# Performance work log

Measured on AMD Instinct MI355X. Metric: run time of the kernel, lower is better.

## Reference

```python
import jax, jax.numpy as jnp
import numpy as np

B, T, DIM = 1, 1024, 1024
H = 8
QLR, KVLR = 768, 512
DNOPE, DROPE, DV = 128, 64, 128
DK = DNOPE + DROPE  # 192
EPS = 1e-5


def _rms(x, w):
    return x * jax.lax.rsqrt(jnp.mean(x * x, axis=-1, keepdims=True) + EPS) * w


def _l2norm(x):
    return x * jax.lax.rsqrt(jnp.sum(x * x, axis=-1, keepdims=True) + 1e-6)


def setup_inputs() -> dict:
    key = jax.random.key(0)
    ks = jax.random.split(key, 12)
    std = 0.02
    rnd = lambda k, shape: (jax.random.normal(k, shape, dtype=jnp.float32) * std)
    return {
        'x': jax.random.normal(ks[0], (B, T, DIM), dtype=jnp.float32),
        'cos': jax.random.normal(ks[1], (T, DROPE), dtype=jnp.float32),
        'sin': jax.random.normal(ks[2], (T, DROPE), dtype=jnp.float32),
        'wq_a': rnd(ks[3], (DIM, QLR)),
        'q_norm_w': jnp.ones((QLR,), dtype=jnp.float32),
        'wq_b': rnd(ks[4], (QLR, H * DK)),
        'wkv_a': rnd(ks[5], (DIM, KVLR + DROPE)),
        'kv_norm_w': jnp.ones((KVLR,), dtype=jnp.float32),
        'wkv_b': rnd(ks[6], (KVLR, H * (DNOPE + DV))),
        'wg_w': rnd(ks[7], (DIM, H * DK)),
        'wg_b': jnp.zeros((H * DK,), dtype=jnp.float32),
        'wb': rnd(ks[8], (DIM, H)),
        'wo': rnd(ks[9], (H * DV, DIM)),
    }


def _kda(q, k, v, g, beta):
    # q,k: [B,T,H,DK]; v: [B,T,H,DV]; g: [B,T,H,DK] (log-decay); beta: [B,T,H]
    q = _l2norm(q) * (DK ** -0.5)
    k = _l2norm(k)
    # time-major for scan
    qs = jnp.moveaxis(q, 1, 0)
    ks_ = jnp.moveaxis(k, 1, 0)
    vs = jnp.moveaxis(v, 1, 0)
    gs = jnp.moveaxis(g, 1, 0)
    bs = jnp.moveaxis(beta, 1, 0)

    def step(S, inp):
        q_t, k_t, v_t, g_t, b_t = inp  # [B,H,DK],[B,H,DK],[B,H,DV],[B,H,DK],[B,H]
        S = S * jnp.exp(g_t)[..., None]                       # per-key-dim decay
        u_t = b_t[..., None] * (v_t - jnp.einsum('bhk,bhkv->bhv', k_t, S))
        S = S + k_t[..., None] * u_t[..., None, :]            # rank-1 delta update
        o_t = jnp.einsum('bhk,bhkv->bhv', q_t, S)
        return S, o_t

    S0 = jnp.zeros((B, H, DK, DV), dtype=q.dtype)
    _, o = jax.lax.scan(step, S0, (qs, ks_, vs, gs, bs))
    return jnp.moveaxis(o, 0, 1)  # [B,T,H,DV]


def reference(x, cos, sin, wq_a, q_norm_w, wq_b, wkv_a, kv_norm_w, wkv_b, wg_w, wg_b, wb, wo):
    # cos/sin are accepted but unused, matching the original forward body.
    q = (_rms(x @ wq_a, q_norm_w) @ wq_b).reshape(B, T, H, DK)
    kv_all = x @ wkv_a
    kv_c, k_pe = kv_all[..., :KVLR], kv_all[..., KVLR:]       # [B,T,KVLR],[B,T,DROPE]
    kv = (_rms(kv_c, kv_norm_w) @ wkv_b).reshape(B, T, H, DNOPE + DV)
    k_nope, v = kv[..., :DNOPE], kv[..., DNOPE:]
    k = jnp.concatenate(
        [k_nope, jnp.broadcast_to(k_pe[:, :, None, :], (B, T, H, DROPE))], axis=-1)
    g = jax.nn.log_sigmoid(x @ wg_w + wg_b).reshape(B, T, H, DK)
    beta = jax.nn.sigmoid(x @ wb).reshape(B, T, H)
    o = _kda(q, k, v, g, beta)
    o = jnp.nan_to_num(o, nan=0.0, posinf=10000.0, neginf=-10000.0)
    return o.reshape(B, T, H * DV) @ wo
```

## Files before the change

### kernel.cpp

```cpp
#include <hip/hip_runtime.h>
#include <hip/hip_bf16.h>
#include <math.h>

#define TT 1024
#define DIM 1024
#define HH 8
#define QLR 768
#define KVLR 512
#define DNOPE 128
#define DROPE 64
#define DV 128
#define DK 192
#define HDK (HH*DK)
#define HKV (HH*(DNOPE+DV))

#define OY   0
#define OQ   3072
#define OC   6144
#define OPL  9984
#define OU   10240
#define OLAM 12288
#define PABLK 12480

typedef __attribute__((ext_vector_type(8))) short short8;
typedef __attribute__((ext_vector_type(4))) float f32x4;

__device__ __forceinline__ unsigned short f2bf_rn(float f) {
    unsigned u = __float_as_uint(f);
    unsigned lsb = (u >> 16) & 1u;
    u += 0x7fffu + lsb;
    return (unsigned short)(u >> 16);
}
__device__ __forceinline__ float bf2f(unsigned short h) {
    return __uint_as_float(((unsigned)h) << 16);
}

__global__ __launch_bounds__(256) void wconv(
    const float* __restrict__ W0, unsigned short* __restrict__ H0,
    unsigned short* __restrict__ L0, int K0, int N0, int T0,
    const float* __restrict__ W1, unsigned short* __restrict__ H1,
    unsigned short* __restrict__ L1, int K1, int N1, int T1,
    const float* __restrict__ W2, unsigned short* __restrict__ H2,
    unsigned short* __restrict__ L2, int K2, int N2, int T2)
{
    __shared__ float Ls[64][65];
    int bx = blockIdx.x;
    const float* W; unsigned short* H; unsigned short* L; int K, N;
    if (bx < T0)           { W = W0; H = H0; L = L0; K = K0; N = N0; }
    else if (bx < T0 + T1) { bx -= T0; W = W1; H = H1; L = L1; K = K1; N = N1; }
    else                   { bx -= T0 + T1; W = W2; H = H2; L = L2; K = K2; N = N2; }

    const int NT = N >> 6;
    const int kt = bx / NT, nt = bx - kt * NT;
    const int k0 = kt * 64, n0 = nt * 64;
    const int tid = threadIdx.x;
    const int r = tid >> 2, c = (tid & 3) * 16;

#pragma unroll
    for (int i = 0; i < 4; i++)
        *(float4*)&Ls[r][c + i * 4] =
            *(const float4*)&W[(size_t)(k0 + r) * N + n0 + c + i * 4];
    __syncthreads();

    const int nr = tid >> 2, kc = (tid & 3) * 16;
    unsigned short hb[16], lb[16];
#pragma unroll
    for (int j = 0; j < 16; j++) {
        float v = Ls[kc + j][nr];
        unsigned short h = f2bf_rn(v);
        hb[j] = h;
        lb[j] = f2bf_rn(v - bf2f(h));
    }
    size_t ob = (size_t)(n0 + nr) * K + k0 + kc;
    *(float4*)&H[ob]     = ((float4*)hb)[0];
    *(float4*)&H[ob + 8] = ((float4*)hb)[1];
    *(float4*)&L[ob]     = ((float4*)lb)[0];
    *(float4*)&L[ob + 8] = ((float4*)lb)[1];
}

__global__ __launch_bounds__(256) void aconv(
    const float* __restrict__ A, unsigned short* __restrict__ H,
    unsigned short* __restrict__ L)
{
    int i = (blockIdx.x * 256 + threadIdx.x) * 8;
    float4 v0 = *(const float4*)&A[i];
    float4 v1 = *(const float4*)&A[i + 4];
    float vv[8] = {v0.x, v0.y, v0.z, v0.w, v1.x, v1.y, v1.z, v1.w};
    unsigned short hb[8], lb[8];
#pragma unroll
    for (int j = 0; j < 8; j++) {
        unsigned short h = f2bf_rn(vv[j]);
        hb[j] = h;
        lb[j] = f2bf_rn(vv[j] - bf2f(h));
    }
    *(float4*)&H[i] = *(float4*)hb;
    *(float4*)&L[i] = *(float4*)lb;
}

__global__ __launch_bounds__(128) void gemm_bt(
    const unsigned short* __restrict__ Ah0, const unsigned short* __restrict__ Al0,
    const unsigned short* __restrict__ Bh0, const unsigned short* __restrict__ Bl0,
    float* __restrict__ C0, int K0, int N0, int T0,
    const unsigned short* __restrict__ Ah1, const unsigned short* __restrict__ Al1,
    const unsigned short* __restrict__ Bh1, const unsigned short* __restrict__ Bl1,
    float* __restrict__ C1, int K1, int N1, int T1,
    const unsigned short* __restrict__ Ah2, const unsigned short* __restrict__ Al2,
    const unsigned short* __restrict__ Bh2, const unsigned short* __restrict__ Bl2,
    float* __restrict__ C2, int K2, int N2, int T2)
{
    __shared__ unsigned short Ahs[64 * 40], Als[64 * 40];
    __shared__ unsigned short Bhs[64 * 40], Bls[64 * 40];

    int bx = blockIdx.x;
    const unsigned short *Ah, *Al, *Bh, *Bl; float* C; int K, N;
    if (bx < T0) {
        Ah = Ah0; Al = Al0; Bh = Bh0; Bl = Bl0; C = C0; K = K0; N = N0;
    } else if (bx < T0 + T1) {
        bx -= T0; Ah = Ah1; Al = Al1; Bh = Bh1; Bl = Bl1; C = C1; K = K1; N = N1;
    } else {
        bx -= T0 + T1; Ah = Ah2; Al = Al2; Bh = Bh2; Bl = Bl2; C = C2; K = K2; N = N2;
    }

    const int tid = threadIdx.x;
    const int w = tid >> 6, l = tid & 63;
    const int q = l >> 4, m16 = l & 15;
    const int bm = blockIdx.y * 64, bn = bx * 64;

    const int c0i = tid * 2, c1i = tid * 2 + 1;
    const int r0 = c0i >> 2, o0 = (c0i & 3) * 8;
    const int r1 = c1i >> 2, o1 = (c1i & 3) * 8;
    const unsigned short* pAh0 = Ah + (size_t)(bm + r0) * K + o0;
    const unsigned short* pAh1 = Ah + (size_t)(bm + r1) * K + o1;
    const unsigned short* pAl0 = Al + (size_t)(bm + r0) * K + o0;
    const unsigned short* pAl1 = Al + (size_t)(bm + r1) * K + o1;
    const unsigned short* pBh0 = Bh + (size_t)(bn + r0) * K + o0;
    const unsigned short* pBh1 = Bh + (size_t)(bn + r1) * K + o1;
    const unsigned short* pBl0 = Bl + (size_t)(bn + r0) * K + o0;
    const unsigned short* pBl1 = Bl + (size_t)(bn + r1) * K + o1;

    f32x4 acc[2][4];
#pragma unroll
    for (int i = 0; i < 2; i++)
#pragma unroll
        for (int j = 0; j < 4; j++)
            acc[i][j] = (f32x4){0.f, 0.f, 0.f, 0.f};

    float4 vAh0 = *(const float4*)pAh0, vAh1 = *(const float4*)pAh1;
    float4 vAl0 = *(const float4*)pAl0, vAl1 = *(const float4*)pAl1;
    float4 vBh0 = *(const float4*)pBh0, vBh1 = *(const float4*)pBh1;
    float4 vBl0 = *(const float4*)pBl0, vBl1 = *(const float4*)pBl1;

    for (int k0 = 0;; k0 += 32) {
        __syncthreads();
        *(float4*)&Ahs[r0 * 40 + o0] = vAh0; *(float4*)&Ahs[r1 * 40 + o1] = vAh1;
        *(float4*)&Als[r0 * 40 + o0] = vAl0; *(float4*)&Als[r1 * 40 + o1] = vAl1;
        *(float4*)&Bhs[r0 * 40 + o0] = vBh0; *(float4*)&Bhs[r1 * 40 + o1] = vBh1;
        *(float4*)&Bls[r0 * 40 + o0] = vBl0; *(float4*)&Bls[r1 * 40 + o1] = vBl1;
        __syncthreads();

        const bool more = (k0 + 32) < K;
        if (more) {
            const int kn = k0 + 32;
            vAh0 = *(const float4*)(pAh0 + kn); vAh1 = *(const float4*)(pAh1 + kn);
            vAl0 = *(const float4*)(pAl0 + kn); vAl1 = *(const float4*)(pAl1 + kn);
            vBh0 = *(const float4*)(pBh0 + kn); vBh1 = *(const float4*)(pBh1 + kn);
            vBl0 = *(const float4*)(pBl0 + kn); vBl1 = *(const float4*)(pBl1 + kn);
        }

        short8 fah[2], fal[2], fbh[4], fbl[4];
#pragma unroll
        for (int mt = 0; mt < 2; mt++) {
            const int row = w * 32 + mt * 16 + m16;
            fah[mt] = *(const short8*)&Ahs[row * 40 + q * 8];
            fal[mt] = *(const short8*)&Als[row * 40 + q * 8];
        }
#pragma unroll
        for (int nt = 0; nt < 4; nt++) {
            const int row = nt * 16 + m16;
            fbh[nt] = *(const short8*)&Bhs[row * 40 + q * 8];
            fbl[nt] = *(const short8*)&Bls[row * 40 + q * 8];
        }
#pragma unroll
        for (int mt = 0; mt < 2; mt++)
#pragma unroll
            for (int nt = 0; nt < 4; nt++) {
                acc[mt][nt] = __builtin_amdgcn_mfma_f32_16x16x32_bf16(
                    fah[mt], fbh[nt], acc[mt][nt], 0, 0, 0);
                acc[mt][nt] = __builtin_amdgcn_mfma_f32_16x16x32_bf16(
                    fah[mt], fbl[nt], acc[mt][nt], 0, 0, 0);
                acc[mt][nt] = __builtin_amdgcn_mfma_f32_16x16x32_bf16(
                    fal[mt], fbh[nt], acc[mt][nt], 0, 0, 0);
            }
        if (!more) break;
    }

#pragma unroll
    for (int mt = 0; mt < 2; mt++)
#pragma unroll
        for (int nt = 0; nt < 4; nt++) {
            const int mrow = bm + w * 32 + mt * 16 + q * 4;
            const int ncol = bn + nt * 16 + m16;
#pragma unroll
            for (int r = 0; r < 4; r++)
                C[(size_t)(mrow + r) * N + ncol] = acc[mt][nt][r];
        }
}

__global__ __launch_bounds__(256) void rmsnorm_bf2(
    const float* __restrict__ in0, const float* __restrict__ w0,
    unsigned short* __restrict__ oh0, unsigned short* __restrict__ ol0,
    const float* __restrict__ in1, const float* __restrict__ w1,
    unsigned short* __restrict__ oh1, unsigned short* __restrict__ ol1)
{
    int bx = blockIdx.x;
    const float* in; const float* w; unsigned short *oh, *ol;
    int t, stride, ncols; float inv_n;
    if (bx < TT) {
        t = bx; in = in0; w = w0; oh = oh0; ol = ol0;
        stride = QLR; ncols = QLR; inv_n = 1.f / QLR;
    } else {
        t = bx - TT; in = in1; w = w1; oh = oh1; ol = ol1;
        stride = KVLR + DROPE; ncols = KVLR; inv_n = 1.f / KVLR;
    }
    const int tid = threadIdx.x;
    const float* row = in + (size_t)t * stride;
    float ss = 0.f;
    for (int c = tid; c < ncols; c += 256) { float v = row[c]; ss += v * v; }
#pragma unroll
    for (int m = 1; m < 64; m <<= 1) ss += __shfl_xor(ss, m);
    __shared__ float red[4];
    if ((tid & 63) == 0) red[tid >> 6] = ss;
    __syncthreads();
    float tot = red[0] + red[1] + red[2] + red[3];
    float scale = rsqrtf(tot * inv_n + 1e-5f);
    for (int c = tid; c < ncols; c += 256) {
        float v = row[c] * scale * w[c];
        unsigned short h = f2bf_rn(v);
        oh[(size_t)t * ncols + c] = h;
        ol[(size_t)t * ncols + c] = f2bf_rn(v - bf2f(h));
    }
}

__global__ __launch_bounds__(256) void small_fused(
    const float* __restrict__ g, const float* __restrict__ bias,
    float* __restrict__ la_h,
    const float* __restrict__ x, const float* __restrict__ wb,
    float* __restrict__ betab,
    const float* __restrict__ qraw, const float* __restrict__ kvb,
    const float* __restrict__ kv_all, float* __restrict__ q_h,
    float* __restrict__ k_h)
{
    int bx = blockIdx.x;
    if (bx < 6144) {
        int i = bx * 256 + threadIdx.x;
        int t = i / HDK, col = i - t * HDK;
        int h = col / DK, d = col - h * DK;
        float z = g[i] + bias[col];
        float la = fminf(z, 0.f) - log1pf(__expf(-fabsf(z)));
        la_h[((size_t)h * TT + t) * DK + d] = la;
        return;
    }
    bx -= 6144;
    const int lane = threadIdx.x & 63, wv = threadIdx.x >> 6;
    if (bx < 2048) {
        const int p = bx * 4 + wv;
        const int t = p >> 3, h = p & 7;
        const float* xr = x + (size_t)t * DIM;
        float s = 0.f;
        for (int e = lane; e < DIM; e += 64) s += xr[e] * wb[e * HH + h];
#pragma unroll
        for (int m = 1; m < 64; m <<= 1) s += __shfl_xor(s, m);
        if (lane == 0) betab[p] = 1.f / (1.f + expf(-s));
        return;
    }
    bx -= 2048;
    {
        const int p = bx * 4 + wv;
        const int t = p >> 3, h = p & 7;

        const float* qrow = qraw + (size_t)t * HDK + h * DK;
        float q0 = qrow[lane], q1 = qrow[lane + 64], q2 = qrow[lane + 128];
        float ss = q0 * q0 + q1 * q1 + q2 * q2;
#pragma unroll
        for (int m = 1; m < 64; m <<= 1) ss += __shfl_xor(ss, m);
        float sc = rsqrtf(ss + 1e-6f) * 0.07216878364870323f;
        float* qo = q_h + ((size_t)h * TT + t) * DK;
        qo[lane] = q0 * sc; qo[lane + 64] = q1 * sc; qo[lane + 128] = q2 * sc;

        const float* knope = kvb + (size_t)t * HKV + h * (DNOPE + DV);
        float k0 = knope[lane], k1 = knope[lane + 64];
        float k2 = kv_all[(size_t)t * (KVLR + DROPE) + KVLR + lane];
        float ks = k0 * k0 + k1 * k1 + k2 * k2;
#pragma unroll
        for (int m = 1; m < 64; m <<= 1) ks += __shfl_xor(ks, m);
        float kc = rsqrtf(ks + 1e-6f);
        float* ko = k_h + ((size_t)h * TT + t) * DK;
        ko[lane] = k0 * kc; ko[lane + 64] = k1 * kc; ko[lane + 128] = k2 * kc;
    }
}

__device__ __forceinline__ float dpp_xor1(float x) {
    return __int_as_float(__builtin_amdgcn_update_dpp(
        0, __float_as_int(x), 0xB1, 0xF, 0xF, false));
}
__device__ __forceinline__ float dpp_xor2(float x) {
    return __int_as_float(__builtin_amdgcn_update_dpp(
        0, __float_as_int(x), 0x4E, 0xF, 0xF, false));
}
__device__ __forceinline__ float dpp_hm(float x) {
    return __int_as_float(__builtin_amdgcn_update_dpp(
        0, __float_as_int(x), 0x141, 0xF, 0xF, false));
}
__device__ __forceinline__ float red16(float x) {
    x += dpp_xor1(x);
    x += dpp_xor2(x);
    x += dpp_hm(x);
    x += __int_as_float(__builtin_amdgcn_update_dpp(0, __float_as_int(x), 0x140, 0xF, 0xF, false));
    return x;
}

__device__ __forceinline__ void gl_lds16(const float* g, float* l) {
    __builtin_amdgcn_global_load_lds(
        (const __attribute__((address_space(1))) void*)g,
        (__attribute__((address_space(3))) void*)l, 16, 0, 0);
}
__device__ __forceinline__ void gl_lds4(const float* g, float* l) {
    __builtin_amdgcn_global_load_lds(
        (const __attribute__((address_space(1))) void*)g,
        (__attribute__((address_space(3))) void*)l, 4, 0, 0);
}

__global__ __launch_bounds__(256) void chunk_prep(
    const float* __restrict__ k_h, const float* __restrict__ la_h,
    const float* __restrict__ q_h, const float* __restrict__ kvb,
    const float* __restrict__ betab, float* __restrict__ pa)
{
    __shared__ float Ls[16][196];
    __shared__ float Ks[16][196];
    __shared__ float Qs[16][196];
    __shared__ float Ws[16][196];
    __shared__ float Xs[16][196];
    __shared__ float Ms[16][16];
    __shared__ float bs[16];

    const int tid = threadIdx.x;
    const int n = blockIdx.x >> 3, h = blockIdx.x & 7;
    const size_t g0 = ((size_t)h * TT + n * 16) * DK;
    float* blob = pa + (size_t)blockIdx.x * PABLK;

#pragma unroll
    for (int s = 0; s < 3; s++) {
        int off = (tid * 3 + s) * 4;
        int r = off / 192, c = off - r * 192;
        *(float4*)&Ks[r][c] = *(const float4*)(k_h + g0 + off);
        *(float4*)&Ls[r][c] = *(const float4*)(la_h + g0 + off);
        *(float4*)&Qs[r][c] = *(const float4*)(q_h + g0 + off);
    }
    if (tid < 16) bs[tid] = betab[(size_t)(n * 16 + tid) * HH + h];
    __syncthreads();

    if (tid < 192) {
        float g = 0.f;
#pragma unroll
        for (int i = 0; i < 16; i++) { g += Ls[i][tid]; Ls[i][tid] = g; }
    }
    __syncthreads();

#pragma unroll
    for (int s = 0; s < 12; s++) {
        int idx = s * 256 + tid;
        int i = idx / 192, d = idx - i * 192;
        float G = Ls[i][d];
        float eg = __expf(G), en = __expf(-G);
        float kk = Ks[i][d];
        Ws[i][d] = bs[i] * kk * eg;
        Qs[i][d] *= eg;
        Ks[i][d] = kk * en;
    }
    __syncthreads();

#pragma unroll
    for (int s = 0; s < 3; s++) {
        int off = (tid * 3 + s) * 4;
        int r = off / 192, c = off - r * 192;
        *(float4*)(blob + OQ + off) = *(const float4*)&Qs[r][c];
    }
    if (tid < 192) {
        float lam = __expf(Ls[15][tid]);
        blob[OLAM + tid] = lam;
#pragma unroll
        for (int j4 = 0; j4 < 4; j4++) {
            float4 v;
            v.x = Ks[j4 * 4 + 0][tid] * lam; v.y = Ks[j4 * 4 + 1][tid] * lam;
            v.z = Ks[j4 * 4 + 2][tid] * lam; v.w = Ks[j4 * 4 + 3][tid] * lam;
            *(float4*)(blob + OC + tid * 20 + j4 * 4) = v;
        }
        blob[OC + tid * 20 + 16] = lam;
        blob[OC + tid * 20 + 17] = 0.f;
        blob[OC + tid * 20 + 18] = 0.f; blob[OC + tid * 20 + 19] = 0.f;
    }
    {
        const int i = tid >> 4, j = tid & 15;
        float m = 0.f, p = 0.f;
#pragma unroll
        for (int d4 = 0; d4 < 48; d4++) {
            float4 w  = *(const float4*)&Ws[i][d4 * 4];
            float4 ka = *(const float4*)&Ks[j][d4 * 4];
            float4 qa = *(const float4*)&Qs[i][d4 * 4];
            m += w.x * ka.x + w.y * ka.y + w.z * ka.z + w.w * ka.w;
            p += qa.x * ka.x + qa.y * ka.y + qa.z * ka.z + qa.w * ka.w;
        }
        Ms[i][j] = (j < i) ? m : 0.f;
        blob[OPL + tid] = (j <= i) ? p : 0.f;
    }
    __syncthreads();

    float y[16], uu[16];
    const bool doY = (tid < 192);
    const bool doU = (tid >= 128);
    const int dcol = tid, ccol = tid - 128;
    if (doY) {
#pragma unroll
        for (int i = 0; i < 16; i++) y[i] = Ws[i][dcol];
#pragma unroll
        for (int i = 1; i < 16; i++)
#pragma unroll
            for (int j = 0; j < i; j++)
                y[i] = fmaf(-Ms[i][j], y[j], y[i]);
    }
    if (doU) {
#pragma unroll
        for (int i = 0; i < 16; i++)
            uu[i] = bs[i] * kvb[(size_t)(n * 16 + i) * HKV + h * (DNOPE + DV) + DNOPE + ccol];
#pragma unroll
        for (int i = 1; i < 16; i++)
#pragma unroll
            for (int j = 0; j < i; j++)
                uu[i] = fmaf(-Ms[i][j], uu[j], uu[i]);
    }
    if (doY) {
#pragma unroll
        for (int i = 0; i < 16; i++) Xs[i][dcol] = y[i];
    }
    __syncthreads();
#pragma unroll
    for (int s = 0; s < 3; s++) {
        int off = (tid * 3 + s) * 4;
        int r = off / 192, c = off - r * 192;
        *(float4*)(blob + OY + off) = *(const float4*)&Xs[r][c];
    }
    __syncthreads();
    if (doU) {
#pragma unroll
        for (int i = 0; i < 16; i++) Xs[i][ccol] = uu[i];
    }
    __syncthreads();
#pragma unroll
    for (int s = 0; s < 2; s++) {
        int off = (tid * 2 + s) * 4;
        int r = off / 128, c = off - r * 128;
        *(float4*)(blob + OU + off) = *(const float4*)&Xs[r][c];
    }
}

__global__ __launch_bounds__(512, 4) void kda_chunk(
    const float* __restrict__ pa, unsigned short* __restrict__ obh,
    unsigned short* __restrict__ obl)
{
    __shared__ float Cb[3][3840];
    __shared__ float Pb[3][256];
    __shared__ float ubs[3][32];
    __shared__ float lbs[3][192];
    __shared__ float Ss[392];
    __shared__ float us[40];

    const int tid = threadIdx.x;
    const int w = tid >> 6, lane = tid & 63;
    const int h = blockIdx.x & 7, cg = blockIdx.x >> 3;
    const int c0 = cg * 2;

    const int dg  = tid & 15;
    const int cc  = (tid >> 4) & 1;
    const int tig = tid >> 5;
    const int dbase = dg * 12;

    auto stage = [&](int buf, int n) {
        const float* blob = pa + (size_t)(n * 8 + h) * PABLK;
        if (w < 3) {
#pragma unroll
            for (int s = 0; s < 4; s++)
                gl_lds16(blob + OC + (w * 4 + s) * 256 + lane * 4,
                         &Cb[buf][(w * 4 + s) * 256]);
        } else if (w == 3) {
#pragma unroll
            for (int s = 12; s < 15; s++)
                gl_lds16(blob + OC + s * 256 + lane * 4, &Cb[buf][s * 256]);
        } else if (w == 4) {
            gl_lds16(blob + OPL + lane * 4, &Pb[buf][0]);
        } else if (w == 5) {
            if (lane < 32)
                gl_lds4(blob + OU + (lane >> 1) * 128 + c0 + (lane & 1), &ubs[buf][0]);
            if (lane < 48)
                gl_lds16(blob + OLAM + lane * 4, &lbs[buf][0]);
        }
    };

    auto ldYQ = [&](int n, float4 (&Y)[3], float4 (&Q)[3]) {
        const float* blob = pa + (size_t)(n * 8 + h) * PABLK;
        const float* py_ = blob + OY + tig * 192 + dbase;
        const float* pq_ = blob + OQ + tig * 192 + dbase;
#pragma unroll
        for (int s = 0; s < 3; s++) {
            Y[s] = *(const float4*)(py_ + s * 4);
            Q[s] = *(const float4*)(pq_ + s * 4);
        }
    };

    for (int idx = tid; idx < 392; idx += 512) Ss[idx] = 0.f;
    stage(0, 0);
    stage(1, 1);

    float4 YA[3], QA[3], YB[3], QB[3];
    ldYQ(0, YA, QA);

    auto body = [&](int n, int bf, float4 (&Yc)[3], float4 (&Qc)[3],
                    float4 (&Yn)[3], float4 (&Qn)[3]) {
        __syncthreads();

        if (n + 2 < TT / 16) {
            int b2 = bf + 2; if (b2 >= 3) b2 -= 3;
            stage(b2, n + 2);
        }
        {
            int np = n + 1; if (np > TT / 16 - 1) np = TT / 16 - 1;
            ldYQ(np, Yn, Qn);
        }

        float4 sv[3];
#pragma unroll
        for (int s = 0; s < 3; s++)
            sv[s] = *(const float4*)&Ss[cc * 196 + dbase + s * 4];

        float py = 0.f, pq = 0.f;
#pragma unroll
        for (int s = 0; s < 3; s++) {
            float4 yv = Yc[s];
            float4 qv = Qc[s];
            float4 s4 = sv[s];
            py = fmaf(yv.x, s4.x, py);
            py = fmaf(yv.y, s4.y, py);
            py = fmaf(yv.z, s4.z, py);
            py = fmaf(yv.w, s4.w, py);
            pq = fmaf(qv.x, s4.x, pq);
            pq = fmaf(qv.y, s4.y, pq);
            pq = fmaf(qv.z, s4.z, pq);
            pq = fmaf(qv.w, s4.w, pq);
        }
        float zy = red16(py);
        float zq = red16(pq);

        float uv = ubs[bf][tig * 2 + cc] - zy;
        if (dg == 0) us[cc * 20 + tig] = uv;
        __syncthreads();

        {
            float acc = (dg <= tig) ? Pb[bf][tig * 16 + dg] * us[cc * 20 + dg]
                                    : 0.f;
            acc = red16(acc);
            if (dg == 0) {
                float ov = zq + acc;
                if (isnan(ov)) ov = 0.f;
                else if (isinf(ov)) ov = ov > 0.f ? 1e4f : -1e4f;
                size_t oi = (size_t)(n * 16 + tig) * (HH * DV) + h * DV + c0 + cc;
                unsigned short hb = f2bf_rn(ov);
                obh[oi] = hb;
                obl[oi] = f2bf_rn(ov - bf2f(hb));
            }
        }

        if (tid < 384) {
            const int d = tid >> 1, c2 = tid & 1;
            const float4* up = (const float4*)&us[c2 * 20];
            float4 u0 = up[0], u1 = up[1], u2v = up[2], u3 = up[3];
            float svv = Ss[c2 * 196 + d];
            float a2 = lbs[bf][d] * svv;
            const float4* C4 = (const float4*)&Cb[bf][d * 20];
            float4 k0 = C4[0], k1 = C4[1], k2 = C4[2], k3 = C4[3];
            a2 = fmaf(k0.x, u0.x,  a2); a2 = fmaf(k0.y, u0.y,  a2);
            a2 = fmaf(k0.z, u0.z,  a2); a2 = fmaf(k0.w, u0.w,  a2);
            a2 = fmaf(k1.x, u1.x,  a2); a2 = fmaf(k1.y, u1.y,  a2);
            a2 = fmaf(k1.z, u1.z,  a2); a2 = fmaf(k1.w, u1.w,  a2);
            a2 = fmaf(k2.x, u2v.x, a2); a2 = fmaf(k2.y, u2v.y, a2);
            a2 = fmaf(k2.z, u2v.z, a2); a2 = fmaf(k2.w, u2v.w, a2);
            a2 = fmaf(k3.x, u3.x,  a2); a2 = fmaf(k3.y, u3.y,  a2);
            a2 = fmaf(k3.z, u3.z,  a2); a2 = fmaf(k3.w, u3.w,  a2);
            Ss[c2 * 196 + d] = a2;
        }
    };

    int buf = 0;
    for (int n = 0; n < TT / 16; n += 2) {
        body(n, buf, YA, QA, YB, QB);
        int b1 = buf + 1; if (b1 >= 3) b1 -= 3;
        body(n + 1, b1, YB, QB, YA, QA);
        buf += 2; if (buf >= 3) buf -= 3;
    }
}

extern "C" void kernel_launch(void* const* d_in, const int* in_sizes, int n_in,
                              void* d_out, int out_size, void* d_ws, size_t ws_size,
                              hipStream_t stream)
{
    const float* x         = (const float*)d_in[0];
    const float* wq_a      = (const float*)d_in[3];
    const float* q_norm_w  = (const float*)d_in[4];
    const float* wq_b      = (const float*)d_in[5];
    const float* wkv_a     = (const float*)d_in[6];
    const float* kv_norm_w = (const float*)d_in[7];
    const float* wkv_b     = (const float*)d_in[8];
    const float* wg_w      = (const float*)d_in[9];
    const float* wg_b      = (const float*)d_in[10];
    const float* wb        = (const float*)d_in[11];
    const float* wo        = (const float*)d_in[12];
    float* out = (float*)d_out;

    float* ws = (float*)d_ws;
    float* xq     = ws;
    float* kv_all = xq     + TT * QLR;
    float* agraw  = kv_all + TT * (KVLR + DROPE);
    float* qnraw  = agraw  + TT * HDK;
    float* kvb    = qnraw  + TT * HDK;
    float* la_h   = kvb    + TT * HKV;
    float* q_h    = la_h   + TT * HDK;
    float* k_h    = q_h    + TT * HDK;
    float* betab  = k_h    + TT * HDK;
    float* pa     = betab  + TT * HH;
    float* tail   = pa     + 512 * PABLK;

    unsigned short* wo_h  = (unsigned short*)tail;
    unsigned short* wo_l  = wo_h  + 1048576;
    unsigned short* xh    = wo_l  + 1048576;
    unsigned short* xl    = xh    + 1048576;
    unsigned short* xqh   = xl    + 1048576;
    unsigned short* xql   = xqh   + 786432;
    unsigned short* kvnh  = xql   + 786432;
    unsigned short* kvnl  = kvnh  + 524288;

    unsigned short* wqa_h  = (unsigned short*)pa;
    unsigned short* wqa_l  = wqa_h  + 786432;
    unsigned short* wkva_h = wqa_l  + 786432;
    unsigned short* wkva_l = wkva_h + 589824;
    unsigned short* wgw_h  = wkva_l + 589824;
    unsigned short* wgw_l  = wgw_h  + 1572864;
    unsigned short* wqb_h  = wgw_l  + 1572864;
    unsigned short* wqb_l  = wqb_h  + 1179648;
    unsigned short* wkvb_h = wqb_l  + 1179648;
    unsigned short* wkvb_l = wkvb_h + 1048576;

    unsigned short* obh = (unsigned short*)agraw;
    unsigned short* obl = obh + 1048576;

    dim3 blk(256);

    wconv<<<dim3(192 + 144 + 384), blk, 0, stream>>>(
        wq_a, wqa_h, wqa_l, DIM, QLR, 192,
        wkv_a, wkva_h, wkva_l, DIM, KVLR + DROPE, 144,
        wg_w, wgw_h, wgw_l, DIM, HDK, 384);
    wconv<<<dim3(288 + 256 + 256), blk, 0, stream>>>(
        wq_b, wqb_h, wqb_l, QLR, HDK, 288,
        wkv_b, wkvb_h, wkvb_l, KVLR, HKV, 256,
        wo, wo_h, wo_l, DIM, DIM, 256);

    aconv<<<dim3(TT * DIM / (256 * 8)), blk, 0, stream>>>(x, xh, xl);

    gemm_bt<<<dim3(12 + 9 + 24, 16), dim3(128), 0, stream>>>(
        xh, xl, wqa_h, wqa_l, xq, DIM, QLR, 12,
        xh, xl, wkva_h, wkva_l, kv_all, DIM, KVLR + DROPE, 9,
        xh, xl, wgw_h, wgw_l, agraw, DIM, HDK, 24);

    rmsnorm_bf2<<<dim3(2 * TT), blk, 0, stream>>>(
        xq, q_norm_w, xqh, xql,
        kv_all, kv_norm_w, kvnh, kvnl);

    gemm_bt<<<dim3(24 + 32, 16), dim3(128), 0, stream>>>(
        xqh, xql, wqb_h, wqb_l, qnraw, QLR, HDK, 24,
        kvnh, kvnl, wkvb_h, wkvb_l, kvb, KVLR, HKV, 32,
        xh, xl, wqa_h, wqa_l, xq, DIM, QLR, 0);

    small_fused<<<dim3(6144 + 2048 + 2048), blk, 0, stream>>>(
        agraw, wg_b, la_h,
        x, wb, betab,
        qnraw, kvb, kv_all, q_h, k_h);

    chunk_prep<<<512, blk, 0, stream>>>(k_h, la_h, q_h, kvb, betab, pa);
    kda_chunk<<<512, dim3(512), 0, stream>>>(pa, obh, obl);

    gemm_bt<<<dim3(16, 16), dim3(128), 0, stream>>>(
        obh, obl, wo_h, wo_l, out, DIM, DIM, 16,
        xh, xl, wqa_h, wqa_l, xq, DIM, QLR, 0,
        xh, xl, wqa_h, wqa_l, xq, DIM, QLR, 0);
}
```

Before: 316.4 us.

## Widen KDA recurrence blocks to four value columns and relayout U blob

Each kda_chunk block now handles four value columns per head with 1024 threads (256 blocks instead of 512), so every staged C/P/lambda chunk in LDS is reused across twice as many columns. The U blob written by chunk_prep is transposed to column-major so each block loads its slice with 16-byte async loads, which also removes two barriers in chunk_prep. The loop body hoists LDS reads ahead of the dot products, splits FMA chains into two accumulators, and replaces __syncthreads with explicit waitcnt+barrier. The trade-off is fewer blocks across the CUs, so the serial 64-step scan gets less parallelism from the block count, and the hand-written barriers rely on correct wait counts.

```diff
diff --git a/kernel.cpp b/kernel.cpp
--- a/kernel.cpp
+++ b/kernel.cpp
@@ -13,6 +13,7 @@
 #define DK 192
 #define HDK (HH*DK)
 #define HKV (HH*(DNOPE+DV))
+#define NBODY (TT/16)
 
 #define OY   0
 #define OQ   3072
@@ -324,11 +325,6 @@
         (const __attribute__((address_space(1))) void*)g,
         (__attribute__((address_space(3))) void*)l, 16, 0, 0);
 }
-__device__ __forceinline__ void gl_lds4(const float* g, float* l) {
-    __builtin_amdgcn_global_load_lds(
-        (const __attribute__((address_space(1))) void*)g,
-        (__attribute__((address_space(3))) void*)l, 4, 0, 0);
-}
 
 __global__ __launch_bounds__(256) void chunk_prep(
     const float* __restrict__ k_h, const float* __restrict__ la_h,
@@ -449,57 +445,49 @@
         int r = off / 192, c = off - r * 192;
         *(float4*)(blob + OY + off) = *(const float4*)&Xs[r][c];
     }
-    __syncthreads();
     if (doU) {
 #pragma unroll
-        for (int i = 0; i < 16; i++) Xs[i][ccol] = uu[i];
-    }
-    __syncthreads();
-#pragma unroll
-    for (int s = 0; s < 2; s++) {
-        int off = (tid * 2 + s) * 4;
-        int r = off / 128, c = off - r * 128;
-        *(float4*)(blob + OU + off) = *(const float4*)&Xs[r][c];
-    }
-}
-
-__global__ __launch_bounds__(512, 4) void kda_chunk(
+        for (int i4 = 0; i4 < 4; i4++) {
+            float4 t;
+            t.x = uu[i4 * 4 + 0]; t.y = uu[i4 * 4 + 1];
+            t.z = uu[i4 * 4 + 2]; t.w = uu[i4 * 4 + 3];
+            *(float4*)(blob + OU + (size_t)ccol * 16 + i4 * 4) = t;
+        }
+    }
+}
+
+__global__ __launch_bounds__(1024) void kda_chunk(
     const float* __restrict__ pa, unsigned short* __restrict__ obh,
     unsigned short* __restrict__ obl)
 {
     __shared__ float Cb[3][3840];
     __shared__ float Pb[3][256];
-    __shared__ float ubs[3][32];
+    __shared__ float ubs[3][64];
     __shared__ float lbs[3][192];
-    __shared__ float Ss[392];
-    __shared__ float us[40];
+    __shared__ float Ss[784];
+    __shared__ float us[80];
 
     const int tid = threadIdx.x;
     const int w = tid >> 6, lane = tid & 63;
     const int h = blockIdx.x & 7, cg = blockIdx.x >> 3;
-    const int c0 = cg * 2;
-
-    const int dg  = tid & 15;
-    const int cc  = (tid >> 4) & 1;
-    const int tig = tid >> 5;
+    const int c0 = cg * 4;
+
+    const int ti  = w;
+    const int cc  = lane >> 4;
+    const int dg  = lane & 15;
     const int dbase = dg * 12;
+
+    const int ud = tid >> 2;
+    const int uc = tid & 3;
 
     auto stage = [&](int buf, int n) {
         const float* blob = pa + (size_t)(n * 8 + h) * PABLK;
-        if (w < 3) {
-#pragma unroll
-            for (int s = 0; s < 4; s++)
-                gl_lds16(blob + OC + (w * 4 + s) * 256 + lane * 4,
-                         &Cb[buf][(w * 4 + s) * 256]);
-        } else if (w == 3) {
-#pragma unroll
-            for (int s = 12; s < 15; s++)
-                gl_lds16(blob + OC + s * 256 + lane * 4, &Cb[buf][s * 256]);
-        } else if (w == 4) {
+        if (w < 15) {
+            gl_lds16(blob + OC + w * 256 + lane * 4, &Cb[buf][w * 256]);
+        } else {
             gl_lds16(blob + OPL + lane * 4, &Pb[buf][0]);
-        } else if (w == 5) {
-            if (lane < 32)
-                gl_lds4(blob + OU + (lane >> 1) * 128 + c0 + (lane & 1), &ubs[buf][0]);
+            if (lane < 16)
+                gl_lds16(blob + OU + c0 * 16 + lane * 4, &ubs[buf][0]);
             if (lane < 48)
                 gl_lds16(blob + OLAM + lane * 4, &lbs[buf][0]);
         }
@@ -507,8 +495,8 @@
 
     auto ldYQ = [&](int n, float4 (&Y)[3], float4 (&Q)[3]) {
         const float* blob = pa + (size_t)(n * 8 + h) * PABLK;
-        const float* py_ = blob + OY + tig * 192 + dbase;
-        const float* pq_ = blob + OQ + tig * 192 + dbase;
+        const float* py_ = blob + OY + ti * 192 + dbase;
+        const float* pq_ = blob + OQ + ti * 192 + dbase;
 #pragma unroll
         for (int s = 0; s < 3; s++) {
             Y[s] = *(const float4*)(py_ + s * 4);
@@ -516,90 +504,101 @@
         }
     };
 
-    for (int idx = tid; idx < 392; idx += 512) Ss[idx] = 0.f;
+    for (int idx = tid; idx < 784; idx += 1024) Ss[idx] = 0.f;
     stage(0, 0);
     stage(1, 1);
 
     float4 YA[3], QA[3], YB[3], QB[3];
     ldYQ(0, YA, QA);
+    asm volatile("s_waitcnt vmcnt(0)" ::: "memory");
 
     auto body = [&](int n, int bf, float4 (&Yc)[3], float4 (&Qc)[3],
                     float4 (&Yn)[3], float4 (&Qn)[3]) {
-        __syncthreads();
-
-        if (n + 2 < TT / 16) {
+        asm volatile("s_waitcnt lgkmcnt(0)\n\ts_barrier" ::: "memory");
+
+        if (n + 2 < NBODY) {
             int b2 = bf + 2; if (b2 >= 3) b2 -= 3;
             stage(b2, n + 2);
         }
+        asm volatile("" ::: "memory");
         {
-            int np = n + 1; if (np > TT / 16 - 1) np = TT / 16 - 1;
+            int np = n + 1; if (np > NBODY - 1) np = NBODY - 1;
             ldYQ(np, Yn, Qn);
         }
 
-        float4 sv[3];
-#pragma unroll
-        for (int s = 0; s < 3; s++)
-            sv[s] = *(const float4*)&Ss[cc * 196 + dbase + s * 4];
-
-        float py = 0.f, pq = 0.f;
-#pragma unroll
-        for (int s = 0; s < 3; s++) {
-            float4 yv = Yc[s];
-            float4 qv = Qc[s];
-            float4 s4 = sv[s];
-            py = fmaf(yv.x, s4.x, py);
-            py = fmaf(yv.y, s4.y, py);
-            py = fmaf(yv.z, s4.z, py);
-            py = fmaf(yv.w, s4.w, py);
-            pq = fmaf(qv.x, s4.x, pq);
-            pq = fmaf(qv.y, s4.y, pq);
-            pq = fmaf(qv.z, s4.z, pq);
-            pq = fmaf(qv.w, s4.w, pq);
-        }
-        float zy = red16(py);
-        float zq = red16(pq);
-
-        float uv = ubs[bf][tig * 2 + cc] - zy;
-        if (dg == 0) us[cc * 20 + tig] = uv;
-        __syncthreads();
-
+        float4 sv0 = *(const float4*)&Ss[cc * 196 + dbase];
+        float4 sv1 = *(const float4*)&Ss[cc * 196 + dbase + 4];
+        float4 sv2 = *(const float4*)&Ss[cc * 196 + dbase + 8];
+        float ubv = ubs[bf][cc * 16 + ti];
+        float pbv = (dg <= ti) ? Pb[bf][ti * 16 + dg] : 0.f;
+
+        float lamv = 0.f, ssv = 0.f;
+        float4 k0, k1, k2, k3;
+        if (tid < 768) {
+            lamv = lbs[bf][ud];
+            ssv  = Ss[uc * 196 + ud];
+            const float4* C4 = (const float4*)&Cb[bf][ud * 20];
+            k0 = C4[0]; k1 = C4[1]; k2 = C4[2]; k3 = C4[3];
+        }
+
+        float py0 = 0.f, py1 = 0.f, pq0 = 0.f, pq1 = 0.f;
         {
-            float acc = (dg <= tig) ? Pb[bf][tig * 16 + dg] * us[cc * 20 + dg]
-                                    : 0.f;
+            float4 yv, qv, s4;
+            yv = Yc[0]; qv = Qc[0]; s4 = sv0;
+            py0 = fmaf(yv.x, s4.x, py0); py1 = fmaf(yv.y, s4.y, py1);
+            py0 = fmaf(yv.z, s4.z, py0); py1 = fmaf(yv.w, s4.w, py1);
+            pq0 = fmaf(qv.x, s4.x, pq0); pq1 = fmaf(qv.y, s4.y, pq1);
+            pq0 = fmaf(qv.z, s4.z, pq0); pq1 = fmaf(qv.w, s4.w, pq1);
+            yv = Yc[1]; qv = Qc[1]; s4 = sv1;
+            py0 = fmaf(yv.x, s4.x, py0); py1 = fmaf(yv.y, s4.y, py1);
+            py0 = fmaf(yv.z, s4.z, py0); py1 = fmaf(yv.w, s4.w, py1);
+            pq0 = fmaf(qv.x, s4.x, pq0); pq1 = fmaf(qv.y, s4.y, pq1);
+            pq0 = fmaf(qv.z, s4.z, pq0); pq1 = fmaf(qv.w, s4.w, pq1);
+            yv = Yc[2]; qv = Qc[2]; s4 = sv2;
+            py0 = fmaf(yv.x, s4.x, py0); py1 = fmaf(yv.y, s4.y, py1);
+            py0 = fmaf(yv.z, s4.z, py0); py1 = fmaf(yv.w, s4.w, py1);
+            pq0 = fmaf(qv.x, s4.x, pq0); pq1 = fmaf(qv.y, s4.y, pq1);
+            pq0 = fmaf(qv.z, s4.z, pq0); pq1 = fmaf(qv.w, s4.w, pq1);
+        }
+        float zy = red16(py0 + py1);
+        float zq = red16(pq0 + pq1);
+
+        float uv = ubv - zy;
+        if (dg == 0) us[cc * 20 + ti] = uv;
+        asm volatile("s_waitcnt lgkmcnt(0)\n\ts_barrier" ::: "memory");
+
+        {
+            float acc = pbv * us[cc * 20 + dg];
             acc = red16(acc);
             if (dg == 0) {
                 float ov = zq + acc;
                 if (isnan(ov)) ov = 0.f;
                 else if (isinf(ov)) ov = ov > 0.f ? 1e4f : -1e4f;
-                size_t oi = (size_t)(n * 16 + tig) * (HH * DV) + h * DV + c0 + cc;
+                size_t oi = (size_t)(n * 16 + ti) * (HH * DV) + h * DV + c0 + cc;
                 unsigned short hb = f2bf_rn(ov);
                 obh[oi] = hb;
                 obl[oi] = f2bf_rn(ov - bf2f(hb));
             }
         }
 
-        if (tid < 384) {
-            const int d = tid >> 1, c2 = tid & 1;
-            const float4* up = (const float4*)&us[c2 * 20];
+        if (tid < 768) {
+            const float4* up = (const float4*)&us[uc * 20];
             float4 u0 = up[0], u1 = up[1], u2v = up[2], u3 = up[3];
-            float svv = Ss[c2 * 196 + d];
-            float a2 = lbs[bf][d] * svv;
-            const float4* C4 = (const float4*)&Cb[bf][d * 20];
-            float4 k0 = C4[0], k1 = C4[1], k2 = C4[2], k3 = C4[3];
-            a2 = fmaf(k0.x, u0.x,  a2); a2 = fmaf(k0.y, u0.y,  a2);
-            a2 = fmaf(k0.z, u0.z,  a2); a2 = fmaf(k0.w, u0.w,  a2);
-            a2 = fmaf(k1.x, u1.x,  a2); a2 = fmaf(k1.y, u1.y,  a2);
-            a2 = fmaf(k1.z, u1.z,  a2); a2 = fmaf(k1.w, u1.w,  a2);
-            a2 = fmaf(k2.x, u2v.x, a2); a2 = fmaf(k2.y, u2v.y, a2);
-            a2 = fmaf(k2.z, u2v.z, a2); a2 = fmaf(k2.w, u2v.w, a2);
-            a2 = fmaf(k3.x, u3.x,  a2); a2 = fmaf(k3.y, u3.y,  a2);
-            a2 = fmaf(k3.z, u3.z,  a2); a2 = fmaf(k3.w, u3.w,  a2);
-            Ss[c2 * 196 + d] = a2;
+            float a0 = lamv * ssv, a1 = 0.f;
+            a0 = fmaf(k0.x, u0.x,  a0); a1 = fmaf(k0.y, u0.y,  a1);
+            a0 = fmaf(k0.z, u0.z,  a0); a1 = fmaf(k0.w, u0.w,  a1);
+            a0 = fmaf(k1.x, u1.x,  a0); a1 = fmaf(k1.y, u1.y,  a1);
+            a0 = fmaf(k1.z, u1.z,  a0); a1 = fmaf(k1.w, u1.w,  a1);
+            a0 = fmaf(k2.x, u2v.x, a0); a1 = fmaf(k2.y, u2v.y, a1);
+            a0 = fmaf(k2.z, u2v.z, a0); a1 = fmaf(k2.w, u2v.w, a1);
+            a0 = fmaf(k3.x, u3.x,  a0); a1 = fmaf(k3.y, u3.y,  a1);
+            a0 = fmaf(k3.z, u3.z,  a0); a1 = fmaf(k3.w, u3.w,  a1);
+            Ss[uc * 196 + ud] = a0 + a1;
         }
     };
 
     int buf = 0;
-    for (int n = 0; n < TT / 16; n += 2) {
+    for (int n = 0; n < NBODY; n += 2) {
         body(n, buf, YA, QA, YB, QB);
         int b1 = buf + 1; if (b1 >= 3) b1 -= 3;
         body(n + 1, b1, YB, QB, YA, QA);
@@ -693,7 +692,7 @@
         qnraw, kvb, kv_all, q_h, k_h);
 
     chunk_prep<<<512, blk, 0, stream>>>(k_h, la_h, q_h, kvb, betab, pa);
-    kda_chunk<<<512, dim3(512), 0, stream>>>(pa, obh, obl);
+    kda_chunk<<<256, dim3(1024), 0, stream>>>(pa, obh, obl);
 
     gemm_bt<<<dim3(16, 16), dim3(128), 0, stream>>>(
         obh, obl, wo_h, wo_l, out, DIM, DIM, 16,
```

Result: no change. 316.2 us (-0.1%).
